# Performance work log

Hardware: AMD Instinct MI355X
Metric: run time of the kernel (lower is better)

Reference implementation:

```python
import jax, jax.numpy as jnp
import numpy as np

C, S, K, SIGMA = 512, 11, 3, 16
B = 128
EPS = 1e-5  # BatchNorm eps (eval mode, running_mean=0, running_var=1)


def _make_dct_weight(Cc, H, W):
    # FcaNet 'low16' frequency selection
    lx = [0, 0, 1, 1, 0, 2, 2, 1, 2, 0, 3, 4, 0, 1, 3, 0]
    ly = [0, 1, 0, 1, 2, 0, 1, 2, 2, 3, 0, 0, 4, 3, 1, 5]
    mx = [u * (H // 7) for u in lx]
    my = [v * (W // 7) for v in ly]
    w = np.zeros((Cc, H, W), np.float32)
    cp = Cc // len(lx)

    def bf(pos, freq, POS):
        r = np.cos(np.pi * freq * (pos + 0.5) / POS) / np.sqrt(POS)
        return r if freq == 0 else r * np.sqrt(2.0)

    for i, (u, v) in enumerate(zip(mx, my)):
        for tx in range(H):
            for ty in range(W):
                w[i * cp:(i + 1) * cp, tx, ty] = bf(tx, u, H) * bf(ty, v, W)
    return jnp.asarray(w)


def _bn(f, g, b):
    # eval-mode BatchNorm2d: (f - 0)/sqrt(1+eps)*g + b, per channel (axis 1)
    s = g / jnp.sqrt(1.0 + EPS)
    return f * s[None, :, None, None] + b[None, :, None, None]


def _conv1x1(f, w, b):
    return jnp.einsum('bchw,oc->bohw', f, w) + b[None, :, None, None]


def _spatial_kernel(f, w_conv, b_conv, g_sp, b_sp):
    Bn = f.shape[0]
    s = _conv1x1(f, w_conv, b_conv)                  # (B, K*K, S, S)
    s = s.reshape(Bn, K * K, S * S).transpose(0, 2, 1)  # (B, S*S, K*K)
    s = _bn(s.reshape(Bn, S * S, K, K), g_sp, b_sp)
    return s.reshape(Bn, S * S, K * K)


def _channel_kernel(f, dct_w, fc1, fc2, g_ch, b_ch):
    y = jnp.sum(f * dct_w[None], axis=(-2, -1))      # (B, C) DCT pooling
    y = jax.nn.sigmoid(jax.nn.relu(y @ fc1.T) @ fc2.T)  # (B, C*K*K)
    y = _bn(y.reshape(-1, C, K, K), g_ch, b_ch)
    return y.reshape(-1, C, K * K)


def _unfold(f):
    # torch-style per-pixel kxk neighborhoods -> (B, C, H, W, K, K)
    p = (K + 1) // 2 - 1
    Bn, Cn, H, W = f.shape
    fp = jnp.pad(f, ((0, 0), (0, 0), (p, p), (p, p)))
    pat = jnp.stack([fp[:, :, di:di + H, dj:dj + W]
                     for di in range(K) for dj in range(K)], axis=-1)
    return pat.reshape(Bn, Cn, H, W, K, K)


def setup_inputs() -> dict:
    key = jax.random.key(0)
    ks = iter(jax.random.split(key, 32))

    def nrm(shape, s=0.02):
        return s * jax.random.normal(next(ks), shape, jnp.float32)

    def gma(shape):
        return 1.0 + 0.1 * jax.random.normal(next(ks), shape, jnp.float32)

    return dict(
        x=jax.random.normal(next(ks), (B, C, S, S), jnp.float32),
        dct_w=_make_dct_weight(C, S, S),
        w_conv=nrm((K * K, C)), b_conv=nrm((K * K,)),
        g_sp=gma((S * S,)), b_sp=nrm((S * S,), 0.05),
        g_ch=gma((C,)), b_ch=nrm((C,), 0.05),
        fc1=nrm((C // SIGMA, C)), fc2=nrm((C * K * K, C // SIGMA)),
        up_w1=nrm((2 * C, C)), up_b1=nrm((2 * C,)), up_g1=gma((2 * C,)), up_bb1=nrm((2 * C,), 0.05),
        up_w2=nrm((2 * C, 2 * C)), up_b2=nrm((2 * C,)), up_g2=gma((2 * C,)), up_bb2=nrm((2 * C,), 0.05),
        lo_w1=nrm((2 * C, 2 * C)), lo_b1=nrm((2 * C,)), lo_g1=gma((2 * C,)), lo_bb1=nrm((2 * C,), 0.05),
        lo_w2=nrm((C, 2 * C)), lo_b2=nrm((C,)), lo_g2=gma((C,)), lo_bb2=nrm((C,), 0.05),
    )


def reference(x, dct_w, w_conv, b_conv, g_sp, b_sp, g_ch, b_ch, fc1, fc2,
              up_w1, up_b1, up_g1, up_bb1, up_w2, up_b2, up_g2, up_bb2,
              lo_w1, lo_b1, lo_g1, lo_bb1, lo_w2, lo_b2, lo_g2, lo_bb2):
    Bn = x.shape[0]
    # instance kernel: spatial (B,1,HW,KK) x channel (B,C,1,KK)
    sk = _spatial_kernel(x, w_conv, b_conv, g_sp, b_sp)[:, None]
    ck = _channel_kernel(x, dct_w, fc1, fc2, g_ch, b_ch)[:, :, None]
    inst = (sk * ck).reshape(Bn, C, S, S, K, K)
    # CLM task representation (sum over batch between upper and lower)
    a = jax.nn.relu(_bn(_conv1x1(x, up_w1, up_b1), up_g1, up_bb1))
    a = jax.nn.relu(_bn(_conv1x1(a, up_w2, up_b2), up_g2, up_bb2))
    a = a.sum(axis=0, keepdims=True)
    a = jax.nn.relu(_bn(_conv1x1(a, lo_w1, lo_b1), lo_g1, lo_bb1))
    task_s = jax.nn.sigmoid(_bn(_conv1x1(a, lo_w2, lo_b2), lo_g2, lo_bb2))
    # task kernel (shared across the batch)
    sk_t = _spatial_kernel(task_s, w_conv, b_conv, g_sp, b_sp)[:, None]
    ck_t = _channel_kernel(task_s, dct_w, fc1, fc2, g_ch, b_ch)[:, :, None]
    task_kernel = (sk_t * ck_t).reshape(1, C, S, S, K, K)
    kernel = task_kernel * inst
    adapted = (_unfold(x) * kernel).mean(axis=(-1, -2))  # (B,C,S,S)
    return adapted + x, task_kernel
```

## Files before the change

### kernel.cpp

```cpp
#include <hip/hip_runtime.h>
#include <hip/hip_bf16.h>
#include <math.h>

#define BNEPS 1e-5f
#define BDIM_B 128
#define CDIM 512
#define SS 121
#define KK 9
#define MROWS (BDIM_B * SS)

typedef unsigned short u16;
typedef __bf16 bf16x8 __attribute__((ext_vector_type(8)));
typedef float f32x4 __attribute__((ext_vector_type(4)));

__device__ __forceinline__ u16 f2bf(float f) {
    union { float f; unsigned int u; } v; v.f = f;
    unsigned int r = v.u + 0x7FFF + ((v.u >> 16) & 1);
    return (u16)(r >> 16);
}
__device__ __forceinline__ float bf2f(u16 v) {
    union { unsigned int u; float f; } x; x.u = ((unsigned int)v) << 16; return x.f;
}

__device__ __forceinline__ void gld16(const u16* g, u16* l) {
    __builtin_amdgcn_global_load_lds(
        (const __attribute__((address_space(1))) void*)g,
        (__attribute__((address_space(3))) void*)l, 16, 0, 0);
}

template<int MODE, int SWIZ>
__global__ __launch_bounds__(256)
void gemm_mfma(const u16* __restrict__ A, const u16* __restrict__ Bw,
               const float* __restrict__ bias, const float* __restrict__ g,
               const float* __restrict__ bb, void* __restrict__ out,
               int Kd, int N, int NT)
{
    __shared__ __align__(16) u16 Als[2][128 * 32];
    __shared__ __align__(16) u16 Bls[2][128 * 32];

    const int tid  = threadIdx.x;
    const int lane = tid & 63;
    const int w    = tid >> 6;
    const int wm   = w >> 1, wn = w & 1;

    int bx, by;
    if (SWIZ) {
        int i = blockIdx.x;
        if (i < 960) {
            int xg = i & 7;
            int j  = i >> 3;
            bx = xg * 15 + (j >> 3);
            by = j & 7;
        } else { bx = 120; by = i - 960; }
    } else {
        bx = blockIdx.x / NT; by = blockIdx.x - bx * NT;
    }
    const int bm = bx * 128;
    const int bn = by * 128;

    f32x4 acc[4][4] = {};

    const int subrow = tid >> 2;
    const int kq     = tid & 3;
    const int gchunk = kq ^ ((subrow >> 1) & 3);
    const u16* Ab = A  + (size_t)(bm + subrow) * Kd + gchunk * 8;
    const u16* Bb = Bw + (size_t)(bn + subrow) * Kd + gchunk * 8;
    u16* Al0  = &Als[0][(w * 16) * 32];
    u16* Al1  = &Als[0][(w * 16 + 64) * 32];
    u16* Bl0  = &Bls[0][(w * 16) * 32];
    u16* Bl1  = &Bls[0][(w * 16 + 64) * 32];
    u16* Al0b = &Als[1][(w * 16) * 32];
    u16* Al1b = &Als[1][(w * 16 + 64) * 32];
    u16* Bl0b = &Bls[1][(w * 16) * 32];
    u16* Bl1b = &Bls[1][(w * 16 + 64) * 32];

    const int fa_row = wm * 64 + (lane & 15);
    const int fb_row = wn * 64 + (lane & 15);
    const int kofs   = (((lane >> 4) ^ (((lane & 15) >> 1) & 3))) * 8;

    for (int k0 = 0; k0 < Kd; k0 += 64) {
        __syncthreads();
        gld16(Ab + k0,                      Al0);
        gld16(Ab + (size_t)64 * Kd + k0,    Al1);
        gld16(Bb + k0,                      Bl0);
        gld16(Bb + (size_t)64 * Kd + k0,    Bl1);
        gld16(Ab + k0 + 32,                 Al0b);
        gld16(Ab + (size_t)64 * Kd + k0 + 32, Al1b);
        gld16(Bb + k0 + 32,                 Bl0b);
        gld16(Bb + (size_t)64 * Kd + k0 + 32, Bl1b);
        __syncthreads();

        #pragma unroll
        for (int hb = 0; hb < 2; ++hb) {
            const u16* Ah = &Als[hb][0];
            const u16* Bh = &Bls[hb][0];
            bf16x8 af[4], bfv[4];
            #pragma unroll
            for (int i = 0; i < 4; ++i)
                af[i] = *(const bf16x8*)&Ah[(fa_row + i * 16) * 32 + kofs];
            #pragma unroll
            for (int j = 0; j < 4; ++j)
                bfv[j] = *(const bf16x8*)&Bh[(fb_row + j * 16) * 32 + kofs];
            #pragma unroll
            for (int i = 0; i < 4; ++i)
                #pragma unroll
                for (int j = 0; j < 4; ++j)
                    acc[i][j] = __builtin_amdgcn_mfma_f32_16x16x32_bf16(af[i], bfv[j], acc[i][j], 0, 0, 0);
        }
    }

    const float inv = 1.0f / sqrtf(1.0f + BNEPS);

    if (MODE == 1) {
        u16* Y = (u16*)out;
        int dstrow[4][4];
        #pragma unroll
        for (int i = 0; i < 4; ++i) {
            int mb = bm + wm * 64 + i * 16 + (lane >> 4) * 4;
            #pragma unroll
            for (int r = 0; r < 4; ++r) {
                int m = mb + r;
                int b = m / 121, p = m - b * 121;
                dstrow[i][r] = p * 128 + b;
            }
        }
        #pragma unroll
        for (int j = 0; j < 4; ++j) {
            int n = bn + wn * 64 + j * 16 + (lane & 15);
            float sc = g[n] * inv, bo = bias[n], bv = bb[n];
            #pragma unroll
            for (int i = 0; i < 4; ++i)
                #pragma unroll
                for (int r = 0; r < 4; ++r) {
                    float v = (acc[i][j][r] + bo) * sc + bv;
                    v = fmaxf(v, 0.0f);
                    Y[(size_t)dstrow[i][r] * N + n] = f2bf(v);
                }
        }
    } else if (MODE == 2) {
        float ps[4];
        #pragma unroll
        for (int j = 0; j < 4; ++j) {
            int n = bn + wn * 64 + j * 16 + (lane & 15);
            float sc = g[n] * inv, bo = bias[n], bv = bb[n];
            float s = 0.f;
            #pragma unroll
            for (int i = 0; i < 4; ++i)
                #pragma unroll
                for (int r = 0; r < 4; ++r) {
                    float v = (acc[i][j][r] + bo) * sc + bv;
                    s += fmaxf(v, 0.0f);
                }
            ps[j] = s;
        }
        __syncthreads();
        float* red = (float*)Als;
        #pragma unroll
        for (int j = 0; j < 4; ++j)
            red[(wm * 4 + (lane >> 4)) * 128 + wn * 64 + j * 16 + (lane & 15)] = ps[j];
        __syncthreads();
        if (tid < 128) {
            float s = 0.f;
            #pragma unroll
            for (int r = 0; r < 8; ++r) s += red[r * 128 + tid];
            ((u16*)out)[(size_t)bx * N + bn + tid] = f2bf(s);
        }
    } else {
        u16* Y = (u16*)out;
        #pragma unroll
        for (int j = 0; j < 4; ++j) {
            int n = bn + wn * 64 + j * 16 + (lane & 15);
            float sc = g[n] * inv, bo = bias[n], bv = bb[n];
            #pragma unroll
            for (int i = 0; i < 4; ++i) {
                int mb = bm + wm * 64 + i * 16 + (lane >> 4) * 4;
                #pragma unroll
                for (int r = 0; r < 4; ++r) {
                    float v = (acc[i][j][r] + bo) * sc + bv;
                    if (MODE == 3) v = fmaxf(v, 0.0f);
                    else           v = 1.f / (1.f + expf(-v));
                    Y[(size_t)(mb + r) * N + n] = f2bf(v);
                }
            }
        }
    }
}

#define W1N (1024 * 512)
#define W2N (1024 * 1024)
#define L1N (1024 * 1024)
#define L2N (512 * 1024)
#define DCTN (512 * 121)
#define WCN (16 * 512)
#define PREP_ELEM (W1N + W2N + L1N + L2N + DCTN + WCN)
#define PREP_BLKS (1024 + (PREP_ELEM + 255) / 256)
__global__ void prep_combo(const float* __restrict__ x, u16* __restrict__ Xb,
                           const float* __restrict__ w1, const float* __restrict__ w2,
                           const float* __restrict__ l1, const float* __restrict__ l2,
                           const float* __restrict__ dct, const float* __restrict__ w_conv,
                           u16* __restrict__ o1, u16* __restrict__ o2,
                           u16* __restrict__ o3, u16* __restrict__ o4,
                           float* __restrict__ dctT, u16* __restrict__ wcb)
{
    __shared__ float t[64 * 121];
    if (blockIdx.x < 1024) {
        int b = blockIdx.x >> 3, c0 = (blockIdx.x & 7) * 64;
        for (int idx = threadIdx.x; idx < 64 * 121; idx += 256) {
            int c = idx / 121, p = idx - c * 121;
            t[idx] = x[((size_t)b * 512 + c0 + c) * 121 + p];
        }
        __syncthreads();
        for (int idx = threadIdx.x; idx < 121 * 64; idx += 256) {
            int p = idx >> 6, c = idx & 63;
            Xb[((size_t)(b * 121 + p)) * 512 + c0 + c] = f2bf(t[c * 121 + p]);
        }
        return;
    }
    int i = (blockIdx.x - 1024) * 256 + threadIdx.x;
    if (i < W1N) { o1[i] = f2bf(w1[i]); return; }
    i -= W1N;
    if (i < W2N) { o2[i] = f2bf(w2[i]); return; }
    i -= W2N;
    if (i < L1N) { o3[i] = f2bf(l1[i]); return; }
    i -= L1N;
    if (i < L2N) { o4[i] = f2bf(l2[i]); return; }
    i -= L2N;
    if (i < DCTN) {
        int p = i >> 9, c = i & 511;
        dctT[i] = dct[(size_t)c * 121 + p];
        return;
    }
    i -= DCTN;
    if (i < WCN) {
        int n = i >> 9, c = i & 511;
        wcb[i] = (n < 9) ? f2bf(w_conv[(size_t)n * 512 + c]) : (u16)0;
    }
}

__global__ __launch_bounds__(256)
void spatial_ck_combo(const u16* __restrict__ Xb, const u16* __restrict__ Xt,
                      const u16* __restrict__ wcb, const float* __restrict__ b_conv,
                      const float* __restrict__ g_sp, const float* __restrict__ b_sp,
                      const float* __restrict__ dctT,
                      const float* __restrict__ fc1, const float* __restrict__ fc2,
                      const float* __restrict__ g_ch, const float* __restrict__ b_ch,
                      float* __restrict__ skb, float* __restrict__ skt,
                      float* __restrict__ ckbuf, float* __restrict__ ck_t)
{
    const float inv = 1.0f / sqrtf(1.0f + BNEPS);

    if (blockIdx.x < 122) {
        const int tid  = threadIdx.x;
        const int lane = tid & 63;
        const int w    = tid >> 6;
        const bool task = (blockIdx.x == 121);
        const u16* Arow = task ? Xt : Xb + (size_t)blockIdx.x * 128 * 512;

        const int fr = lane & 15;
        const int kq = lane >> 4;
        const int r0 = w * 32;

        f32x4 acc0 = {}, acc1 = {};
        const u16* a0p = Arow + (size_t)(r0 + fr) * 512 + kq * 8;
        const u16* a1p = Arow + (size_t)(r0 + 16 + fr) * 512 + kq * 8;
        const u16* bp  = wcb + (size_t)fr * 512 + kq * 8;
        #pragma unroll
        for (int k0 = 0; k0 < 512; k0 += 32) {
            bf16x8 a0 = *(const bf16x8*)(a0p + k0);
            bf16x8 a1 = *(const bf16x8*)(a1p + k0);
            bf16x8 b  = *(const bf16x8*)(bp + k0);
            acc0 = __builtin_amdgcn_mfma_f32_16x16x32_bf16(a0, b, acc0, 0, 0, 0);
            acc1 = __builtin_amdgcn_mfma_f32_16x16x32_bf16(a1, b, acc1, 0, 0, 0);
        }

        int n = lane & 15;
        if (n < 9) {
            float bo = b_conv[n];
            #pragma unroll
            for (int t = 0; t < 2; ++t) {
                f32x4 a = t ? acc1 : acc0;
                #pragma unroll
                for (int r = 0; r < 4; ++r) {
                    int mloc = r0 + t * 16 + (lane >> 4) * 4 + r;
                    if (!task) {
                        int m = blockIdx.x * 128 + mloc;
                        int p = m % 121;
                        float v = (a[r] + bo) * (g_sp[p] * inv) + b_sp[p];
                        skb[(size_t)m * 9 + n] = v;
                    } else if (mloc < 121) {
                        float v = (a[r] + bo) * (g_sp[mloc] * inv) + b_sp[mloc];
                        skt[(size_t)mloc * 9 + n] = v;
                    }
                }
            }
        }
        return;
    }

    __shared__ float yls[512];
    __shared__ float y2ls[32];
    const int g = blockIdx.x - 122;
    const u16* src = (g < 128) ? Xb + (size_t)g * 121 * 512 : Xt;

    for (int c = threadIdx.x; c < 512; c += 256) {
        float s = 0.f;
        for (int p = 0; p < SS; ++p)
            s += bf2f(src[(size_t)p * 512 + c]) * dctT[p * 512 + c];
        yls[c] = s;
    }
    __syncthreads();

    {
        int o = threadIdx.x >> 3, kp = threadIdx.x & 7;
        const float* w = fc1 + (size_t)o * 512;
        float s = 0.f;
        for (int k = kp * 4; k < 512; k += 32) {
            float4 wv = *(const float4*)(w + k);
            float4 av = *(const float4*)(yls + k);
            s += wv.x * av.x + wv.y * av.y + wv.z * av.z + wv.w * av.w;
        }
        s += __shfl_xor(s, 1);
        s += __shfl_xor(s, 2);
        s += __shfl_xor(s, 4);
        if (kp == 0) y2ls[o] = fmaxf(s, 0.f);
    }
    __syncthreads();

    for (int o = threadIdx.x; o < CDIM * KK; o += 256) {
        const float* w = fc2 + (size_t)o * 32;
        float s = 0.f;
        #pragma unroll
        for (int k = 0; k < 32; ++k) s += y2ls[k] * w[k];
        s = 1.f / (1.f + expf(-s));
        int c = o / KK;
        s = s * (g_ch[c] * inv) + b_ch[c];
        if (g < 128) ckbuf[(size_t)g * CDIM * KK + o] = s;
        else         ck_t[o] = s;
    }
}

#define TKN (CDIM * SS * KK)
#define FIN_BLKS (1024 + (TKN + 255) / 256)
__global__ __launch_bounds__(256)
void final_combo(const float* __restrict__ x, const float* __restrict__ skb,
                 const float* __restrict__ sk_t, const float* __restrict__ ckbuf,
                 const float* __restrict__ ck_t, float* __restrict__ out0,
                 float* __restrict__ tk)
{
    __shared__ float PS[SS * KK];
    __shared__ float CS[64 * KK];
    __shared__ float XT[64 * SS];

    if (blockIdx.x >= 1024) {
        int idx = (blockIdx.x - 1024) * 256 + threadIdx.x;
        if (idx < TKN) {
            int k9 = idx % KK;
            int pc = idx / KK;
            int p = pc % SS, c = pc / SS;
            tk[idx] = sk_t[p * KK + k9] * ck_t[c * KK + k9];
        }
        return;
    }

    const int tid = threadIdx.x;
    const int b = blockIdx.x >> 3, c0 = (blockIdx.x & 7) * 64;

    const float* sp = skb + (size_t)b * SS * KK;
    for (int i = tid; i < SS * KK; i += 256) PS[i] = sp[i] * sk_t[i];
    const float* cp = ckbuf + ((size_t)b * CDIM + c0) * KK;
    const float* tp = ck_t + (size_t)c0 * KK;
    for (int i = tid; i < 64 * KK; i += 256) CS[i] = cp[i] * tp[i];
    const float* xp = x + ((size_t)b * CDIM + c0) * SS;
    for (int i = tid; i < 64 * SS; i += 256) XT[i] = xp[i];
    __syncthreads();

    float* op = out0 + ((size_t)b * CDIM + c0) * SS;
    for (int i = tid; i < 64 * SS; i += 256) {
        int c = i / SS, p = i - c * SS;
        int h = p / 11, w = p - h * 11;
        const float* xc = XT + c * SS;
        const float* ps = PS + p * KK;
        const float* cs = CS + c * KK;
        float acc = 0.f;
        #pragma unroll
        for (int di = 0; di < 3; ++di) {
            int hh = h + di - 1;
            bool hv = (unsigned)hh < 11u;
            #pragma unroll
            for (int dj = 0; dj < 3; ++dj) {
                int ww = w + dj - 1;
                int k = di * 3 + dj;
                float xv = (hv && (unsigned)ww < 11u) ? xc[hh * 11 + ww] : 0.f;
                acc += xv * ps[k] * cs[k];
            }
        }
        op[i] = acc * (1.0f / 9.0f) + xc[p];
    }
}

extern "C" void kernel_launch(void* const* d_in, const int* in_sizes, int n_in,
                              void* d_out, int out_size, void* d_ws, size_t ws_size,
                              hipStream_t stream)
{
    const float* x      = (const float*)d_in[0];
    const float* dct_w  = (const float*)d_in[1];
    const float* w_conv = (const float*)d_in[2];
    const float* b_conv = (const float*)d_in[3];
    const float* g_sp   = (const float*)d_in[4];
    const float* b_sp   = (const float*)d_in[5];
    const float* g_ch   = (const float*)d_in[6];
    const float* b_ch   = (const float*)d_in[7];
    const float* fc1    = (const float*)d_in[8];
    const float* fc2    = (const float*)d_in[9];
    const float* up_w1  = (const float*)d_in[10];
    const float* up_b1  = (const float*)d_in[11];
    const float* up_g1  = (const float*)d_in[12];
    const float* up_bb1 = (const float*)d_in[13];
    const float* up_w2  = (const float*)d_in[14];
    const float* up_b2  = (const float*)d_in[15];
    const float* up_g2  = (const float*)d_in[16];
    const float* up_bb2 = (const float*)d_in[17];
    const float* lo_w1  = (const float*)d_in[18];
    const float* lo_b1  = (const float*)d_in[19];
    const float* lo_g1  = (const float*)d_in[20];
    const float* lo_bb1 = (const float*)d_in[21];
    const float* lo_w2  = (const float*)d_in[22];
    const float* lo_b2  = (const float*)d_in[23];
    const float* lo_g2  = (const float*)d_in[24];
    const float* lo_bb2 = (const float*)d_in[25];

    float* out0 = (float*)d_out;
    float* tk   = out0 + (size_t)BDIM_B * CDIM * SS;

    char* ws = (char*)d_ws;
    size_t off = 0;
    auto alloc = [&](size_t bytes) { void* p = ws + off; off += (bytes + 63) & ~(size_t)63; return p; };
    u16*   Xb      = (u16*)alloc((size_t)MROWS * 512 * 2);
    u16*   Y1      = (u16*)alloc((size_t)MROWS * 1024 * 2);
    u16*   w1b     = (u16*)alloc((size_t)W1N * 2);
    u16*   w2b     = (u16*)alloc((size_t)W2N * 2);
    u16*   lw1b    = (u16*)alloc((size_t)L1N * 2);
    u16*   lw2b    = (u16*)alloc((size_t)L2N * 2);
    u16*   asum_b  = (u16*)alloc((size_t)128 * 1024 * 2);
    u16*   a3b     = (u16*)alloc((size_t)128 * 1024 * 2);
    u16*   ts_pc   = (u16*)alloc((size_t)128 * 512 * 2);
    float* dctT    = (float*)alloc((size_t)SS * 512 * 4);
    u16*   wcb     = (u16*)alloc((size_t)WCN * 2);
    float* ckbuf   = (float*)alloc((size_t)BDIM_B * CDIM * KK * 4);
    float* skbuf   = (float*)alloc((size_t)BDIM_B * SS * KK * 4);
    float* ck_t    = (float*)alloc((size_t)CDIM * KK * 4);
    float* sk_t    = (float*)alloc((size_t)SS * KK * 4);

    hipLaunchKernelGGL(prep_combo, dim3(PREP_BLKS), dim3(256), 0, stream,
                       x, Xb, up_w1, up_w2, lo_w1, lo_w2, dct_w, w_conv,
                       w1b, w2b, lw1b, lw2b, dctT, wcb);

    hipLaunchKernelGGL((gemm_mfma<1, 1>), dim3(121 * 8), dim3(256), 0, stream,
                       Xb, w1b, up_b1, up_g1, up_bb1, (void*)Y1, 512, 1024, 8);
    hipLaunchKernelGGL((gemm_mfma<2, 1>), dim3(121 * 8), dim3(256), 0, stream,
                       Y1, w2b, up_b2, up_g2, up_bb2, (void*)asum_b, 1024, 1024, 8);

    hipLaunchKernelGGL((gemm_mfma<3, 0>), dim3(8), dim3(256), 0, stream,
                       asum_b, lw1b, lo_b1, lo_g1, lo_bb1, (void*)a3b, 1024, 1024, 8);
    hipLaunchKernelGGL((gemm_mfma<4, 0>), dim3(4), dim3(256), 0, stream,
                       a3b, lw2b, lo_b2, lo_g2, lo_bb2, (void*)ts_pc, 1024, 512, 4);

    hipLaunchKernelGGL(spatial_ck_combo, dim3(122 + 129), dim3(256), 0, stream,
                       Xb, ts_pc, wcb, b_conv, g_sp, b_sp,
                       dctT, fc1, fc2, g_ch, b_ch,
                       skbuf, sk_t, ckbuf, ck_t);

    hipLaunchKernelGGL(final_combo, dim3(FIN_BLKS), dim3(256), 0, stream,
                       x, skbuf, sk_t, ckbuf, ck_t, out0, tk);
}
```

Measured before the change: 318.3 us.

## Replace upper CLM GEMMs with 256x256-tile, 4-stage pipelined MFMA kernel

```diff
diff --git a/kernel.cpp b/kernel.cpp
--- a/kernel.cpp
+++ b/kernel.cpp
@@ -26,6 +26,160 @@
     __builtin_amdgcn_global_load_lds(
         (const __attribute__((address_space(1))) void*)g,
         (__attribute__((address_space(3))) void*)l, 16, 0, 0);
+}
+
+__device__ __forceinline__ void wgbar() {
+    asm volatile("" ::: "memory");
+    __builtin_amdgcn_s_barrier();
+    asm volatile("" ::: "memory");
+}
+
+template<int MODE>
+__global__ __launch_bounds__(512, 2)
+void gemm256(const u16* __restrict__ A, const u16* __restrict__ Bw,
+             const float* __restrict__ bias, const float* __restrict__ g,
+             const float* __restrict__ bb, void* __restrict__ out,
+             int Kd, int N, int Mvalid)
+{
+    __shared__ __align__(16) u16 As[4][256 * 32];
+    __shared__ __align__(16) u16 Bs[4][256 * 32];
+
+    const int tid  = threadIdx.x;
+    const int lane = tid & 63;
+    const int w    = tid >> 6;
+    const int wm   = w >> 2;
+    const int wn   = w & 3;
+
+    const int MP   = (Mvalid + 255) >> 8;
+    const int xcd  = blockIdx.x & 7;
+    const int tt   = blockIdx.x >> 3;
+    const int pnl  = (tt >> 2) * 8 + xcd;
+    const int bnid = tt & 3;
+    if (pnl >= MP) return;
+    const int bm = pnl * 256;
+    const int bn = bnid * 256;
+
+    const int srow   = tid >> 2;
+    const int schunk = (tid & 3) ^ ((srow >> 1) & 3);
+    int ar0 = bm + srow;        if (ar0 >= Mvalid) ar0 = Mvalid - 1;
+    int ar1 = bm + 128 + srow;  if (ar1 >= Mvalid) ar1 = Mvalid - 1;
+    const u16* a0 = A  + (size_t)ar0 * Kd + schunk * 8;
+    const u16* a1 = A  + (size_t)ar1 * Kd + schunk * 8;
+    const u16* b0 = Bw + (size_t)(bn + srow) * Kd + schunk * 8;
+    const u16* b1 = Bw + (size_t)(bn + 128 + srow) * Kd + schunk * 8;
+
+#define STAGE_A(S_, T_) do { \
+    gld16(a0 + (T_) * 32, &As[(S_)][(w * 16) * 32]); \
+    gld16(a1 + (T_) * 32, &As[(S_)][(128 + w * 16) * 32]); \
+} while (0)
+#define STAGE_B(S_, T_) do { \
+    gld16(b0 + (T_) * 32, &Bs[(S_)][(w * 16) * 32]); \
+    gld16(b1 + (T_) * 32, &Bs[(S_)][(128 + w * 16) * 32]); \
+} while (0)
+
+    const int frA = wm * 128 + (lane & 15);
+    const int frB = wn * 64  + (lane & 15);
+    const int rch = ((lane >> 4) ^ (((lane & 15) >> 1) & 3)) * 8;
+
+    f32x4 acc[8][4] = {};
+
+    const int NT = Kd >> 5;
+
+    STAGE_A(0, 0); STAGE_B(0, 0);
+    asm volatile("" ::: "memory");
+    STAGE_A(1, 1); STAGE_B(1, 1);
+    asm volatile("" ::: "memory");
+    STAGE_A(2, 2); STAGE_B(2, 2);
+    asm volatile("s_waitcnt vmcnt(8)" ::: "memory");
+    wgbar();
+
+#define TILE(T_, DOSTAGE_, VMW_) do { \
+    const int sl_ = (T_) & 3; \
+    bf16x8 af_[8], bv_[4]; \
+    _Pragma("unroll") \
+    for (int i_ = 0; i_ < 4; ++i_) \
+        af_[i_] = *(const bf16x8*)&As[sl_][(frA + i_ * 16) * 32 + rch]; \
+    _Pragma("unroll") \
+    for (int j_ = 0; j_ < 4; ++j_) \
+        bv_[j_] = *(const bf16x8*)&Bs[sl_][(frB + j_ * 16) * 32 + rch]; \
+    if (DOSTAGE_) STAGE_A(((T_) + 3) & 3, (T_) + 3); \
+    wgbar(); \
+    __builtin_amdgcn_s_setprio(1); \
+    _Pragma("unroll") \
+    for (int i_ = 0; i_ < 4; ++i_) \
+        _Pragma("unroll") \
+        for (int j_ = 0; j_ < 4; ++j_) \
+            acc[i_][j_] = __builtin_amdgcn_mfma_f32_16x16x32_bf16(af_[i_], bv_[j_], acc[i_][j_], 0, 0, 0); \
+    __builtin_amdgcn_s_setprio(0); \
+    wgbar(); \
+    _Pragma("unroll") \
+    for (int i_ = 4; i_ < 8; ++i_) \
+        af_[i_] = *(const bf16x8*)&As[sl_][(frA + i_ * 16) * 32 + rch]; \
+    if (DOSTAGE_) STAGE_B(((T_) + 3) & 3, (T_) + 3); \
+    wgbar(); \
+    __builtin_amdgcn_s_setprio(1); \
+    _Pragma("unroll") \
+    for (int i_ = 4; i_ < 8; ++i_) \
+        _Pragma("unroll") \
+        for (int j_ = 0; j_ < 4; ++j_) \
+            acc[i_][j_] = __builtin_amdgcn_mfma_f32_16x16x32_bf16(af_[i_], bv_[j_], acc[i_][j_], 0, 0, 0); \
+    __builtin_amdgcn_s_setprio(0); \
+    if ((VMW_) == 8)      asm volatile("s_waitcnt vmcnt(8)" ::: "memory"); \
+    else if ((VMW_) == 4) asm volatile("s_waitcnt vmcnt(4)" ::: "memory"); \
+    else if ((VMW_) == 0) asm volatile("s_waitcnt vmcnt(0)" ::: "memory"); \
+    wgbar(); \
+} while (0)
+
+    for (int t = 0; t + 3 < NT; ++t)
+        TILE(t, true, 8);
+    TILE(NT - 3, false, 4);
+    TILE(NT - 2, false, 0);
+    TILE(NT - 1, false, -1);
+
+#undef TILE
+#undef STAGE_A
+#undef STAGE_B
+
+    const float inv = 1.0f / sqrtf(1.0f + BNEPS);
+
+    if (MODE == 1) {
+        u16* Y = (u16*)out;
+        #pragma unroll
+        for (int j = 0; j < 4; ++j) {
+            int n = bn + wn * 64 + j * 16 + (lane & 15);
+            float sc = g[n] * inv, bo = bias[n], bvv = bb[n];
+            #pragma unroll
+            for (int i = 0; i < 8; ++i) {
+                int mb = bm + wm * 128 + i * 16 + (lane >> 4) * 4;
+                #pragma unroll
+                for (int r = 0; r < 4; ++r) {
+                    int m = mb + r;
+                    if (m < Mvalid) {
+                        int b = m / 121, p = m - b * 121;
+                        float v = (acc[i][j][r] + bo) * sc + bvv;
+                        Y[(size_t)(p * 128 + b) * N + n] = f2bf(fmaxf(v, 0.0f));
+                    }
+                }
+            }
+        }
+    } else {
+        int p = pnl * 2 + wm;
+        #pragma unroll
+        for (int j = 0; j < 4; ++j) {
+            int n = bn + wn * 64 + j * 16 + (lane & 15);
+            float sc = g[n] * inv, bo = bias[n], bvv = bb[n];
+            float s = 0.f;
+            #pragma unroll
+            for (int i = 0; i < 8; ++i)
+                #pragma unroll
+                for (int r = 0; r < 4; ++r)
+                    s += fmaxf((acc[i][j][r] + bo) * sc + bvv, 0.0f);
+            s += __shfl_xor(s, 16);
+            s += __shfl_xor(s, 32);
+            if (p < SS && lane < 16)
+                ((u16*)out)[(size_t)p * N + n] = f2bf(s);
+        }
+    }
 }
 
 template<int MODE, int SWIZ>
@@ -455,10 +609,10 @@
                        x, Xb, up_w1, up_w2, lo_w1, lo_w2, dct_w, w_conv,
                        w1b, w2b, lw1b, lw2b, dctT, wcb);
 
-    hipLaunchKernelGGL((gemm_mfma<1, 1>), dim3(121 * 8), dim3(256), 0, stream,
-                       Xb, w1b, up_b1, up_g1, up_bb1, (void*)Y1, 512, 1024, 8);
-    hipLaunchKernelGGL((gemm_mfma<2, 1>), dim3(121 * 8), dim3(256), 0, stream,
-                       Y1, w2b, up_b2, up_g2, up_bb2, (void*)asum_b, 1024, 1024, 8);
+    hipLaunchKernelGGL((gemm256<1>), dim3(256), dim3(512), 0, stream,
+                       Xb, w1b, up_b1, up_g1, up_bb1, (void*)Y1, 512, 1024, MROWS);
+    hipLaunchKernelGGL((gemm256<2>), dim3(256), dim3(512), 0, stream,
+                       Y1, w2b, up_b2, up_g2, up_bb2, (void*)asum_b, 1024, 1024, MROWS);
 
     hipLaunchKernelGGL((gemm_mfma<3, 0>), dim3(8), dim3(256), 0, stream,
                        asum_b, lw1b, lo_b1, lo_g1, lo_bb1, (void*)a3b, 1024, 1024, 8);
```

New measurement: 330.8 us. +3.9%, slower.
